# Performance work log

Hardware: AMD Instinct MI355X
Metric: run time of the kernel (lower is better)

Reference implementation:

```python
import jax, jax.numpy as jnp
import numpy as np

NUM_EXPERTS = 8
RANK = 16
TOP_K = 2
SCALING = 32.0 / RANK  # alpha / rank = 2.0
IN_F = 2048
OUT_F = 2048


def setup_inputs() -> dict:
    key = jax.random.key(0)
    k1, k2, k3, k4, k5 = jax.random.split(key, 5)
    B, T = 4, 2048
    x = jax.random.normal(k1, (B, T, IN_F), dtype=jnp.float32)
    # kaiming-uniform-ish scales
    bound_w = 1.0 / np.sqrt(IN_F)
    weight = jax.random.uniform(k2, (OUT_F, IN_F), jnp.float32, -bound_w, bound_w)
    lora_A = jax.random.uniform(k3, (NUM_EXPERTS, RANK, IN_F), jnp.float32, -bound_w, bound_w)
    # lora_B is zero-initialized in the module; use small random values so the
    # expert path is numerically non-trivial for kernel correctness testing.
    lora_B = 0.02 * jax.random.normal(k4, (NUM_EXPERTS, OUT_F, RANK), dtype=jnp.float32)
    router_w = jax.random.uniform(k5, (NUM_EXPERTS, IN_F), jnp.float32, -bound_w, bound_w)
    return {"x": x, "weight": weight, "lora_A": lora_A, "lora_B": lora_B, "router_w": router_w}


def reference(x, weight, lora_A, lora_B, router_w):
    B, T, D = x.shape
    N = B * T
    # base dense projection: [B,T,O]
    base = jnp.einsum('btd,od->bto', x, weight)
    # routing
    logits = jnp.einsum('btd,ed->bte', x, router_w)
    probs = jax.nn.softmax(logits, axis=-1)
    topk_vals, topk_idx = jax.lax.top_k(probs, TOP_K)          # [B,T,K]
    topk_vals = topk_vals / topk_vals.sum(axis=-1, keepdims=True)
    # dense per-token expert weights: zero for non-selected experts -> same math
    # as the per-k gather loop (top_k indices are distinct).
    w_dense = jnp.zeros((N, NUM_EXPERTS), dtype=x.dtype).at[
        jnp.arange(N)[:, None], topk_idx.reshape(N, TOP_K)
    ].set(topk_vals.reshape(N, TOP_K))                          # [N,E]
    x_flat = x.reshape(N, D)
    # low-rank expert path: Ax [N,E,r] is tiny (E*r=128), then weighted combine
    Ax = jnp.einsum('nd,erd->ner', x_flat, lora_A)
    expert_out = jnp.einsum('ner,ne,eor->no', Ax, w_dense, lora_B) * SCALING
    return base + expert_out.reshape(B, T, OUT_F)
```

## Files before the change

### kernel.cpp

```cpp
#include <hip/hip_runtime.h>
#include <hip/hip_bf16.h>
#include <stdint.h>

#define IN_F   2048
#define OUT_F  2048
#define NTOK   8192
#define KAUG   2176
#define RANKE  128
#define SCALING 2.0f
#define NT_MAIN 34

typedef float  f32x4 __attribute__((ext_vector_type(4)));
typedef __bf16 bf16x8 __attribute__((ext_vector_type(8)));

#define GLOAD(g, l) __builtin_amdgcn_global_load_lds(                                   \
    (const __attribute__((address_space(1))) unsigned int*)(g),                          \
    (__attribute__((address_space(3))) unsigned int*)(l), 16, 0, 0)
#define PIN()    asm volatile("" ::: "memory")
#define BAR()    __builtin_amdgcn_s_barrier()
#define WAITL()  asm volatile("s_waitcnt lgkmcnt(0)" ::: "memory")
#define WAITV0() asm volatile("s_waitcnt vmcnt(0)" ::: "memory")
#define WAITV5() asm volatile("s_waitcnt vmcnt(5)" ::: "memory")
#define WAITV8() asm volatile("s_waitcnt vmcnt(8)" ::: "memory")
#define SB0()    __builtin_amdgcn_sched_barrier(0)

__device__ __forceinline__ unsigned short f2b(float f) {
  union { float f; unsigned u; } v; v.f = f;
  return (unsigned short)((v.u + 0x7FFFu + ((v.u >> 16) & 1u)) >> 16);
}

__device__ __forceinline__ uint4 pack8(float4 a, float4 b) {
  uint4 p;
  p.x = f2b(a.x) | ((unsigned)f2b(a.y) << 16);
  p.y = f2b(a.z) | ((unsigned)f2b(a.w) << 16);
  p.z = f2b(b.x) | ((unsigned)f2b(b.y) << 16);
  p.w = f2b(b.z) | ((unsigned)f2b(b.w) << 16);
  return p;
}

__global__ __launch_bounds__(256)
void k_pre(const float* __restrict__ x, const float* __restrict__ rw,
           const float* __restrict__ wt, const float* __restrict__ lb,
           const float* __restrict__ la,
           unsigned short* __restrict__ Ap, float* __restrict__ wsc,
           unsigned short* __restrict__ Bp, unsigned short* __restrict__ Ac) {
  const int bid = blockIdx.x;
  const int t = threadIdx.x;

  if (bid >= 4096) {
    const int r0 = (bid - 4096) * 16;
    #pragma unroll
    for (int j = 0; j < 16; ++j) {
      int ch = j * 256 + t;
      int row = r0 + (ch >> 8), col8 = ch & 255;
      const float4* src = (const float4*)(la + (size_t)row * IN_F + col8 * 8);
      *(uint4*)(Ac + (size_t)row * IN_F + col8 * 8) = pack8(src[0], src[1]);
    }
    return;
  }
  if (bid >= 2048) {
    const int o = bid - 2048;
    const int c = t * 8;
    const float4* src = (const float4*)(wt + (size_t)o * IN_F + c);
    *(uint4*)(Bp + (size_t)o * KAUG + c) = pack8(src[0], src[1]);
    if (t < RANKE) {
      float v = lb[((size_t)(t >> 4) * OUT_F + o) * 16 + (t & 15)];
      Bp[(size_t)o * KAUG + IN_F + t] = f2b(v);
    }
    return;
  }

  const int w = t >> 6, l = t & 63;
  const int n0 = bid * 4;
  {
    const int n = n0 + w;
    const float4* src = (const float4*)(x + (size_t)n * IN_F);
    uint4* dst = (uint4*)(Ap + (size_t)n * KAUG);
    #pragma unroll
    for (int j = 0; j < 4; ++j) {
      int ch = j * 64 + l;
      dst[ch] = pack8(src[2 * ch], src[2 * ch + 1]);
    }
  }
  const int e = t & 7, p = t >> 3;
  float4 wreg[16];
  {
    const float4* wp = (const float4*)(rw + (size_t)e * IN_F + p * 64);
    #pragma unroll
    for (int j = 0; j < 16; ++j) wreg[j] = wp[j];
  }
  float s[4];
  #pragma unroll
  for (int ti = 0; ti < 4; ++ti) {
    const float4* xp = (const float4*)(x + (size_t)(n0 + ti) * IN_F + p * 64);
    float acc = 0.f;
    #pragma unroll
    for (int j = 0; j < 16; ++j) {
      float4 a = xp[j], b = wreg[j];
      acc += a.x * b.x + a.y * b.y + a.z * b.z + a.w * b.w;
    }
    s[ti] = acc;
  }
  #pragma unroll
  for (int ti = 0; ti < 4; ++ti) {
    s[ti] += __shfl_xor(s[ti], 8);
    s[ti] += __shfl_xor(s[ti], 16);
    s[ti] += __shfl_xor(s[ti], 32);
  }
  __shared__ float red[4][4][8];
  if (l < 8) {
    #pragma unroll
    for (int ti = 0; ti < 4; ++ti) red[ti][w][l] = s[ti];
  }
  __syncthreads();
  if (l < 8) {
    float tot = red[w][0][l] + red[w][1][l] + red[w][2][l] + red[w][3][l];
    float m = tot;
    m = fmaxf(m, __shfl_xor(m, 1));
    m = fmaxf(m, __shfl_xor(m, 2));
    m = fmaxf(m, __shfl_xor(m, 4));
    float ex = expf(tot - m);
    float dn = ex;
    dn += __shfl_xor(dn, 1);
    dn += __shfl_xor(dn, 2);
    dn += __shfl_xor(dn, 4);
    float prob = ex / dn;
    float v1 = prob; int i1 = l;
    #pragma unroll
    for (int msk = 1; msk <= 4; msk <<= 1) {
      float ov = __shfl_xor(v1, msk); int oi = __shfl_xor(i1, msk);
      if (ov > v1 || (ov == v1 && oi < i1)) { v1 = ov; i1 = oi; }
    }
    float v2 = (l == i1) ? -1.f : prob; int i2 = l;
    #pragma unroll
    for (int msk = 1; msk <= 4; msk <<= 1) {
      float ov = __shfl_xor(v2, msk); int oi = __shfl_xor(i2, msk);
      if (ov > v2 || (ov == v2 && oi < i2)) { v2 = ov; i2 = oi; }
    }
    float wsum = v1 + v2;
    float wv = (l == i1) ? (v1 / wsum) : ((l == i2) ? (v2 / wsum) : 0.f);
    wsc[(size_t)(n0 + w) * 8 + l] = wv * SCALING;
  }
}

__global__ __launch_bounds__(256)
void k_lora(const unsigned short* __restrict__ Ap, const unsigned short* __restrict__ Ac,
            const float* __restrict__ wsc, unsigned short* __restrict__ Vout) {
  __shared__ alignas(16) unsigned short LA[3 * 2048];
  __shared__ alignas(16) unsigned short LB[3 * 8192];
  const int t = threadIdx.x, bm = blockIdx.x;
  const int w = t >> 6, l = t & 63;
  const int lr = l & 15, lq = l >> 4, lx = l & 7;
  const unsigned short* Ablk = Ap + (size_t)bm * 32 * KAUG;
  const int rr = t >> 3, cs = t & 7;
  const int sc = cs ^ (rr & 7);

  f32x4 acc[2][2];
  #pragma unroll
  for (int i = 0; i < 2; ++i)
    #pragma unroll
    for (int j = 0; j < 2; ++j) acc[i][j] = f32x4{0.f, 0.f, 0.f, 0.f};

  auto stg = [&](int buf, int kt) {
    GLOAD(Ablk + (size_t)rr * KAUG + kt * 64 + sc * 8, LA + buf * 2048 + w * 512);
    #pragma unroll
    for (int r = 0; r < 4; ++r)
      GLOAD(Ac + (size_t)(r * 32 + rr) * IN_F + kt * 64 + sc * 8,
            LB + buf * 8192 + r * 2048 + w * 512);
  };

  const int as0 = (lq ^ lx) * 8, as1 = ((4 + lq) ^ lx) * 8;

  stg(0, 0); stg(1, 1);
  for (int kt = 0; kt < 32; ++kt) {
    if (kt == 31) { WAITV0(); } else { WAITV5(); }
    PIN(); BAR();
    if (kt + 2 < 32) stg((kt + 2) % 3, kt + 2);
    const int buf = kt % 3;
    bf16x8 aF[2][2], bF[2][2];
    #pragma unroll
    for (int mi = 0; mi < 2; ++mi) {
      aF[mi][0] = *(const bf16x8*)(LA + buf * 2048 + lr * 64 + mi * 1024 + as0);
      aF[mi][1] = *(const bf16x8*)(LA + buf * 2048 + lr * 64 + mi * 1024 + as1);
    }
    #pragma unroll
    for (int ni = 0; ni < 2; ++ni) {
      bF[ni][0] = *(const bf16x8*)(LB + buf * 8192 + w * 2048 + lr * 64 + ni * 1024 + as0);
      bF[ni][1] = *(const bf16x8*)(LB + buf * 8192 + w * 2048 + lr * 64 + ni * 1024 + as1);
    }
    #pragma unroll
    for (int mi = 0; mi < 2; ++mi)
      #pragma unroll
      for (int ni = 0; ni < 2; ++ni)
        #pragma unroll
        for (int ks = 0; ks < 2; ++ks)
          acc[mi][ni] = __builtin_amdgcn_mfma_f32_16x16x32_bf16(aF[mi][ks], bF[ni][ks], acc[mi][ni], 0, 0, 0);
  }

  #pragma unroll
  for (int mi = 0; mi < 2; ++mi)
    #pragma unroll
    for (int ni = 0; ni < 2; ++ni)
      #pragma unroll
      for (int j = 0; j < 4; ++j) {
        int row = bm * 32 + mi * 16 + lq * 4 + j;
        int col = w * 32 + ni * 16 + lr;
        float sg = wsc[row * 8 + (col >> 4)];
        Vout[(size_t)row * KAUG + col] = f2b(acc[mi][ni][j] * sg);
      }
}

__global__ __launch_bounds__(512, 2)
void k_main(const unsigned short* __restrict__ A, const unsigned short* __restrict__ B,
            float* __restrict__ out) {
  __shared__ alignas(16) unsigned short LDS[65536];

  const int tid = threadIdx.x;
  const int id = blockIdx.x;
  const int wg = (id & 7) * 32 + (id >> 3);
  const int bn = wg >> 5, bm = wg & 31;
  const int w = tid >> 6, l = tid & 63;
  const int wr = w >> 2, wc = w & 3;
  const int lr = l & 15, lq = l >> 4, lx = l & 7;

  const unsigned short* Ablk = A + (size_t)bm * 256 * KAUG;
  const unsigned short* Bblk = B + (size_t)bn * 256 * KAUG;

  const int rr = tid >> 3, cs = tid & 7;
  const int sc = cs ^ (rr & 7);
  const size_t gOfs = (size_t)rr * KAUG + sc * 8;
  unsigned short* const ldsW = LDS + w * 512;

  const int aoff = wr * 8192 + lr * 64;
  const int boff = (wc >> 1) * 8192 + (wc & 1) * 4096 + lr * 64;
  const int as0 = (lq ^ lx) * 8, as1 = ((4 + lq) ^ lx) * 8;

  f32x4 acc[8][4];
  #pragma unroll
  for (int i = 0; i < 8; ++i)
    #pragma unroll
    for (int j = 0; j < 4; ++j) acc[i][j] = f32x4{0.f, 0.f, 0.f, 0.f};
  bf16x8 aF[8][2], bF[4][2];

  auto stg = [&](int op, int buf, int h, int kt) {
    const unsigned short* g = (op ? Bblk : Ablk) + (size_t)(h * 128) * KAUG + (size_t)kt * 64 + gOfs;
    unsigned short* ld = ldsW + op * 32768 + buf * 16384 + h * 8192;
    GLOAD(g, ld);
    GLOAD(g + (size_t)64 * KAUG, ld + 4096);
  };

#define QUAD(mq, nq)                                                                     \
  do {                                                                                   \
    _Pragma("unroll") for (int mi_ = 0; mi_ < 4; ++mi_)                                  \
    _Pragma("unroll") for (int ni_ = 0; ni_ < 2; ++ni_)                                  \
    _Pragma("unroll") for (int ks_ = 0; ks_ < 2; ++ks_)                                  \
      acc[(mq)*4 + mi_][(nq)*2 + ni_] = __builtin_amdgcn_mfma_f32_16x16x32_bf16(         \
          aF[(mq)*4 + mi_][ks_], bF[(nq)*2 + ni_][ks_], acc[(mq)*4 + mi_][(nq)*2 + ni_], \
          0, 0, 0);                                                                      \
  } while (0)

  stg(0, 0, 0, 0); stg(0, 0, 1, 0); stg(1, 0, 0, 0); stg(1, 0, 1, 0);
  stg(0, 1, 0, 1); stg(0, 1, 1, 1); stg(1, 1, 0, 1); stg(1, 1, 1, 1);
  WAITV8(); PIN(); BAR();

  for (int t = 0; t < NT_MAIN; ++t) {
    const int buf = t & 1;
    #pragma unroll
    for (int mi = 0; mi < 4; ++mi) {
      aF[mi][0] = *(const bf16x8*)(LDS + buf * 16384 + aoff + mi * 1024 + as0);
      aF[mi][1] = *(const bf16x8*)(LDS + buf * 16384 + aoff + mi * 1024 + as1);
    }
    #pragma unroll
    for (int ni = 0; ni < 2; ++ni) {
      bF[ni][0] = *(const bf16x8*)(LDS + 32768 + buf * 16384 + boff + ni * 1024 + as0);
      bF[ni][1] = *(const bf16x8*)(LDS + 32768 + buf * 16384 + boff + ni * 1024 + as1);
    }
    PIN(); BAR(); WAITL(); SB0();
    __builtin_amdgcn_s_setprio(1); QUAD(0, 0); __builtin_amdgcn_s_setprio(0);
    PIN(); BAR();
    #pragma unroll
    for (int mi = 4; mi < 8; ++mi) {
      aF[mi][0] = *(const bf16x8*)(LDS + buf * 16384 + aoff + mi * 1024 + as0);
      aF[mi][1] = *(const bf16x8*)(LDS + buf * 16384 + aoff + mi * 1024 + as1);
    }
    #pragma unroll
    for (int ni = 2; ni < 4; ++ni) {
      bF[ni][0] = *(const bf16x8*)(LDS + 32768 + buf * 16384 + boff + ni * 1024 + as0);
      bF[ni][1] = *(const bf16x8*)(LDS + 32768 + buf * 16384 + boff + ni * 1024 + as1);
    }
    PIN(); BAR(); WAITL(); SB0();
    __builtin_amdgcn_s_setprio(1); QUAD(0, 1); __builtin_amdgcn_s_setprio(0);
    PIN(); BAR();
    if (t + 2 < NT_MAIN) { stg(0, buf, 0, t + 2); stg(1, buf, 0, t + 2); }
    PIN();
    __builtin_amdgcn_s_setprio(1); QUAD(1, 1); __builtin_amdgcn_s_setprio(0);
    PIN(); BAR();
    if (t + 2 < NT_MAIN) { stg(0, buf, 1, t + 2); stg(1, buf, 1, t + 2); }
    PIN();
    __builtin_amdgcn_s_setprio(1); QUAD(1, 0); __builtin_amdgcn_s_setprio(0);
    if (t + 2 < NT_MAIN) { WAITV8(); } else { WAITV0(); }
    PIN(); BAR();
  }
#undef QUAD

  #pragma unroll
  for (int mi = 0; mi < 8; ++mi)
    #pragma unroll
    for (int ni = 0; ni < 4; ++ni)
      #pragma unroll
      for (int j = 0; j < 4; ++j) {
        int row = bm * 256 + wr * 128 + mi * 16 + lq * 4 + j;
        int col = bn * 256 + wc * 64 + ni * 16 + lr;
        out[(size_t)row * OUT_F + col] = acc[mi][ni][j];
      }
}

extern "C" void kernel_launch(void* const* d_in, const int* in_sizes, int n_in,
                              void* d_out, int out_size, void* d_ws, size_t ws_size,
                              hipStream_t stream) {
  const float* x  = (const float*)d_in[0];
  const float* wt = (const float*)d_in[1];
  const float* la = (const float*)d_in[2];
  const float* lb = (const float*)d_in[3];
  const float* rw = (const float*)d_in[4];
  float* out = (float*)d_out;
  char* ws = (char*)d_ws;

  unsigned short* Ap  = (unsigned short*)ws;
  unsigned short* Bp  = (unsigned short*)(ws + 35651584);
  unsigned short* Ac  = (unsigned short*)(ws + 44564480);
  float*          wsc = (float*)(ws + 45088768);

  k_pre<<<4104, 256, 0, stream>>>(x, rw, wt, lb, la, Ap, wsc, Bp, Ac);
  k_lora<<<NTOK / 32, 256, 0, stream>>>(Ap, Ac, wsc, Ap + IN_F);
  k_main<<<256, 512, 0, stream>>>(Ap, Bp, out);
}
```

Measured before the change: 138.8 us.

## Switch main GEMM to K=32 tiles with four-stage LDS ring buffer

Restructures the main GEMM loop to use 32-wide K tiles instead of 64, with a 4-slot LDS ring buffer and prefetch depth of 3 instead of double-buffered 64-wide tiles. The LDS swizzle and global-to-LDS staging layout change to match the narrower tiles, and A/B loads are split across two phases per iteration. The aim is deeper latency hiding of global loads. In exchange the loop runs twice as many iterations, each with two barriers and fewer MFMAs per barrier, so synchronisation overhead grows.

Measured after the change: 142.9 us. +2.9%, slower.

```diff
diff --git a/kernel.cpp b/kernel.cpp
--- a/kernel.cpp
+++ b/kernel.cpp
@@ -8,7 +8,7 @@
 #define KAUG   2176
 #define RANKE  128
 #define SCALING 2.0f
-#define NT_MAIN 34
+#define NT32   68
 
 typedef float  f32x4 __attribute__((ext_vector_type(4)));
 typedef __bf16 bf16x8 __attribute__((ext_vector_type(8)));
@@ -20,6 +20,7 @@
 #define BAR()    __builtin_amdgcn_s_barrier()
 #define WAITL()  asm volatile("s_waitcnt lgkmcnt(0)" ::: "memory")
 #define WAITV0() asm volatile("s_waitcnt vmcnt(0)" ::: "memory")
+#define WAITV4() asm volatile("s_waitcnt vmcnt(4)" ::: "memory")
 #define WAITV5() asm volatile("s_waitcnt vmcnt(5)" ::: "memory")
 #define WAITV8() asm volatile("s_waitcnt vmcnt(8)" ::: "memory")
 #define SB0()    __builtin_amdgcn_sched_barrier(0)
@@ -221,88 +222,71 @@
   const int bn = wg >> 5, bm = wg & 31;
   const int w = tid >> 6, l = tid & 63;
   const int wr = w >> 2, wc = w & 3;
-  const int lr = l & 15, lq = l >> 4, lx = l & 7;
+  const int lr = l & 15;
 
   const unsigned short* Ablk = A + (size_t)bm * 256 * KAUG;
   const unsigned short* Bblk = B + (size_t)bn * 256 * KAUG;
 
-  const int rr = tid >> 3, cs = tid & 7;
-  const int sc = cs ^ (rr & 7);
-  const size_t gOfs = (size_t)rr * KAUG + sc * 8;
-  unsigned short* const ldsW = LDS + w * 512;
-
-  const int aoff = wr * 8192 + lr * 64;
-  const int boff = (wc >> 1) * 8192 + (wc & 1) * 4096 + lr * 64;
-  const int as0 = (lq ^ lx) * 8, as1 = ((4 + lq) ^ lx) * 8;
+  const int rr = tid >> 2, cs = tid & 3;
+  const size_t gOfs = (size_t)rr * KAUG + (size_t)((cs ^ ((rr >> 1) & 3)) * 8);
+
+  const int slotx = (l >> 4) ^ ((lr >> 1) & 3);
+  const int abase = (wr * 128 + lr) * 32 + slotx * 8;
+  const int bbase = 32768 + (wc * 64 + lr) * 32 + slotx * 8;
 
   f32x4 acc[8][4];
   #pragma unroll
   for (int i = 0; i < 8; ++i)
     #pragma unroll
     for (int j = 0; j < 4; ++j) acc[i][j] = f32x4{0.f, 0.f, 0.f, 0.f};
-  bf16x8 aF[8][2], bF[4][2];
-
-  auto stg = [&](int op, int buf, int h, int kt) {
-    const unsigned short* g = (op ? Bblk : Ablk) + (size_t)(h * 128) * KAUG + (size_t)kt * 64 + gOfs;
-    unsigned short* ld = ldsW + op * 32768 + buf * 16384 + h * 8192;
+  bf16x8 aF[8], bF[4];
+
+  auto stg = [&](int op, int bufm, int h, int kt) {
+    const unsigned short* g = (op ? Bblk : Ablk) + (size_t)(h * 128) * KAUG + (size_t)kt * 32 + gOfs;
+    unsigned short* ld = LDS + op * 32768 + bufm * 8192 + h * 4096 + w * 512;
     GLOAD(g, ld);
-    GLOAD(g + (size_t)64 * KAUG, ld + 4096);
   };
-
-#define QUAD(mq, nq)                                                                     \
-  do {                                                                                   \
-    _Pragma("unroll") for (int mi_ = 0; mi_ < 4; ++mi_)                                  \
-    _Pragma("unroll") for (int ni_ = 0; ni_ < 2; ++ni_)                                  \
-    _Pragma("unroll") for (int ks_ = 0; ks_ < 2; ++ks_)                                  \
-      acc[(mq)*4 + mi_][(nq)*2 + ni_] = __builtin_amdgcn_mfma_f32_16x16x32_bf16(         \
-          aF[(mq)*4 + mi_][ks_], bF[(nq)*2 + ni_][ks_], acc[(mq)*4 + mi_][(nq)*2 + ni_], \
-          0, 0, 0);                                                                      \
-  } while (0)
 
   stg(0, 0, 0, 0); stg(0, 0, 1, 0); stg(1, 0, 0, 0); stg(1, 0, 1, 0);
   stg(0, 1, 0, 1); stg(0, 1, 1, 1); stg(1, 1, 0, 1); stg(1, 1, 1, 1);
+  stg(0, 2, 0, 2); stg(0, 2, 1, 2); stg(1, 2, 0, 2); stg(1, 2, 1, 2);
   WAITV8(); PIN(); BAR();
 
-  for (int t = 0; t < NT_MAIN; ++t) {
-    const int buf = t & 1;
-    #pragma unroll
-    for (int mi = 0; mi < 4; ++mi) {
-      aF[mi][0] = *(const bf16x8*)(LDS + buf * 16384 + aoff + mi * 1024 + as0);
-      aF[mi][1] = *(const bf16x8*)(LDS + buf * 16384 + aoff + mi * 1024 + as1);
-    }
-    #pragma unroll
-    for (int ni = 0; ni < 2; ++ni) {
-      bF[ni][0] = *(const bf16x8*)(LDS + 32768 + buf * 16384 + boff + ni * 1024 + as0);
-      bF[ni][1] = *(const bf16x8*)(LDS + 32768 + buf * 16384 + boff + ni * 1024 + as1);
-    }
+  for (int t = 0; t < NT32; ++t) {
+    const int buf = t & 3, sb = (t + 3) & 3;
+    const int ab = buf * 8192 + abase, bb = buf * 8192 + bbase;
+    #pragma unroll
+    for (int mi = 0; mi < 4; ++mi) aF[mi] = *(const bf16x8*)(LDS + ab + mi * 512);
+    #pragma unroll
+    for (int ni = 0; ni < 4; ++ni) bF[ni] = *(const bf16x8*)(LDS + bb + ni * 512);
+    if (t + 3 < NT32) { stg(0, sb, 0, t + 3); stg(0, sb, 1, t + 3); }
     PIN(); BAR(); WAITL(); SB0();
-    __builtin_amdgcn_s_setprio(1); QUAD(0, 0); __builtin_amdgcn_s_setprio(0);
+    __builtin_amdgcn_s_setprio(1);
+    #pragma unroll
+    for (int mi = 0; mi < 4; ++mi)
+      #pragma unroll
+      for (int ni = 0; ni < 4; ++ni)
+        acc[mi][ni] = __builtin_amdgcn_mfma_f32_16x16x32_bf16(aF[mi], bF[ni], acc[mi][ni], 0, 0, 0);
+    __builtin_amdgcn_s_setprio(0);
     PIN(); BAR();
     #pragma unroll
-    for (int mi = 4; mi < 8; ++mi) {
-      aF[mi][0] = *(const bf16x8*)(LDS + buf * 16384 + aoff + mi * 1024 + as0);
-      aF[mi][1] = *(const bf16x8*)(LDS + buf * 16384 + aoff + mi * 1024 + as1);
-    }
-    #pragma unroll
-    for (int ni = 2; ni < 4; ++ni) {
-      bF[ni][0] = *(const bf16x8*)(LDS + 32768 + buf * 16384 + boff + ni * 1024 + as0);
-      bF[ni][1] = *(const bf16x8*)(LDS + 32768 + buf * 16384 + boff + ni * 1024 + as1);
-    }
+    for (int mi = 4; mi < 8; ++mi) aF[mi] = *(const bf16x8*)(LDS + ab + mi * 512);
+    if (t + 3 < NT32) { stg(1, sb, 0, t + 3); stg(1, sb, 1, t + 3); }
     PIN(); BAR(); WAITL(); SB0();
-    __builtin_amdgcn_s_setprio(1); QUAD(0, 1); __builtin_amdgcn_s_setprio(0);
+    __builtin_amdgcn_s_setprio(1);
+    #pragma unroll
+    for (int mi = 4; mi < 8; ++mi)
+      #pragma unroll
+      for (int ni = 0; ni < 4; ++ni)
+        acc[mi][ni] = __builtin_amdgcn_mfma_f32_16x16x32_bf16(aF[mi], bF[ni], acc[mi][ni], 0, 0, 0);
+    __builtin_amdgcn_s_setprio(0);
+    if (t + 3 < NT32) { WAITV8(); }
+    else if (t + 2 < NT32) { WAITV4(); }
+    else if (t + 1 < NT32) { WAITV0(); }
     PIN(); BAR();
-    if (t + 2 < NT_MAIN) { stg(0, buf, 0, t + 2); stg(1, buf, 0, t + 2); }
-    PIN();
-    __builtin_amdgcn_s_setprio(1); QUAD(1, 1); __builtin_amdgcn_s_setprio(0);
-    PIN(); BAR();
-    if (t + 2 < NT_MAIN) { stg(0, buf, 1, t + 2); stg(1, buf, 1, t + 2); }
-    PIN();
-    __builtin_amdgcn_s_setprio(1); QUAD(1, 0); __builtin_amdgcn_s_setprio(0);
-    if (t + 2 < NT_MAIN) { WAITV8(); } else { WAITV0(); }
-    PIN(); BAR();
-  }
-#undef QUAD
-
+  }
+
+  const int lq = l >> 4;
   #pragma unroll
   for (int mi = 0; mi < 8; ++mi)
     #pragma unroll
```

## Restructure GEMM pipeline with staggered A/B prefetch and reduced fragment registers

Applied to the files above, without the earlier changes.

The main bf16 GEMM loop is unrolled by two k-tiles and reschedules the global-to-LDS loads. A halves for the next tile are issued early within the current tile, and B halves two tiles ahead. A fragments are reloaded per M-quad so only four A fragments are live, which cuts register pressure. The pre-kernel also folds the x-to-bf16 conversion into the router dot-product loop so x is read once instead of twice. The tighter buffer reuse depends on the barrier and waitcnt ordering being correct, so a misplaced wait could race on LDS.

Result: slower. 195.4 us (+40.7%).

```diff
diff --git a/kernel.cpp b/kernel.cpp
--- a/kernel.cpp
+++ b/kernel.cpp
@@ -8,7 +8,8 @@
 #define KAUG   2176
 #define RANKE  128
 #define SCALING 2.0f
-#define NT_MAIN 34
+#define NT64   34
+#define NITER  17
 
 typedef float  f32x4 __attribute__((ext_vector_type(4)));
 typedef __bf16 bf16x8 __attribute__((ext_vector_type(8)));
@@ -19,9 +20,10 @@
 #define PIN()    asm volatile("" ::: "memory")
 #define BAR()    __builtin_amdgcn_s_barrier()
 #define WAITL()  asm volatile("s_waitcnt lgkmcnt(0)" ::: "memory")
+#define WAITL8() asm volatile("s_waitcnt lgkmcnt(8)" ::: "memory")
 #define WAITV0() asm volatile("s_waitcnt vmcnt(0)" ::: "memory")
+#define WAITV4() asm volatile("s_waitcnt vmcnt(4)" ::: "memory")
 #define WAITV5() asm volatile("s_waitcnt vmcnt(5)" ::: "memory")
-#define WAITV8() asm volatile("s_waitcnt vmcnt(8)" ::: "memory")
 #define SB0()    __builtin_amdgcn_sched_barrier(0)
 
 __device__ __forceinline__ unsigned short f2b(float f) {
@@ -72,16 +74,6 @@
 
   const int w = t >> 6, l = t & 63;
   const int n0 = bid * 4;
-  {
-    const int n = n0 + w;
-    const float4* src = (const float4*)(x + (size_t)n * IN_F);
-    uint4* dst = (uint4*)(Ap + (size_t)n * KAUG);
-    #pragma unroll
-    for (int j = 0; j < 4; ++j) {
-      int ch = j * 64 + l;
-      dst[ch] = pack8(src[2 * ch], src[2 * ch + 1]);
-    }
-  }
   const int e = t & 7, p = t >> 3;
   float4 wreg[16];
   {
@@ -93,11 +85,15 @@
   #pragma unroll
   for (int ti = 0; ti < 4; ++ti) {
     const float4* xp = (const float4*)(x + (size_t)(n0 + ti) * IN_F + p * 64);
+    uint4* dst = (uint4*)(Ap + (size_t)(n0 + ti) * KAUG + p * 64);
     float acc = 0.f;
+    float4 prev;
     #pragma unroll
     for (int j = 0; j < 16; ++j) {
       float4 a = xp[j], b = wreg[j];
       acc += a.x * b.x + a.y * b.y + a.z * b.z + a.w * b.w;
+      if (j & 1) { if (e == ti) dst[j >> 1] = pack8(prev, a); }
+      else prev = a;
     }
     s[ti] = acc;
   }
@@ -226,79 +222,124 @@
   const unsigned short* Ablk = A + (size_t)bm * 256 * KAUG;
   const unsigned short* Bblk = B + (size_t)bn * 256 * KAUG;
 
-  const int rr = tid >> 3, cs = tid & 7;
-  const int sc = cs ^ (rr & 7);
-  const size_t gOfs = (size_t)rr * KAUG + sc * 8;
+  const size_t gofs0 = (size_t)(tid >> 3) * KAUG + (size_t)(((tid & 7) ^ ((tid >> 3) & 7)) * 8);
+  const size_t gofs1 = (size_t)((tid + 512) >> 3) * KAUG +
+                       (size_t)((((tid + 512) & 7) ^ (((tid + 512) >> 3) & 7)) * 8);
   unsigned short* const ldsW = LDS + w * 512;
 
-  const int aoff = wr * 8192 + lr * 64;
-  const int boff = (wc >> 1) * 8192 + (wc & 1) * 4096 + lr * 64;
-  const int as0 = (lq ^ lx) * 8, as1 = ((4 + lq) ^ lx) * 8;
+  const int arow = wr * 128 + lr, brow = wc * 64 + lr;
+  const int sl0 = (lq ^ lx) * 8, sl1 = ((4 + lq) ^ lx) * 8;
 
   f32x4 acc[8][4];
   #pragma unroll
   for (int i = 0; i < 8; ++i)
     #pragma unroll
     for (int j = 0; j < 4; ++j) acc[i][j] = f32x4{0.f, 0.f, 0.f, 0.f};
-  bf16x8 aF[8][2], bF[4][2];
-
-  auto stg = [&](int op, int buf, int h, int kt) {
-    const unsigned short* g = (op ? Bblk : Ablk) + (size_t)(h * 128) * KAUG + (size_t)kt * 64 + gOfs;
-    unsigned short* ld = ldsW + op * 32768 + buf * 16384 + h * 8192;
-    GLOAD(g, ld);
-    GLOAD(g + (size_t)64 * KAUG, ld + 4096);
+  bf16x8 aF[4][2], bF[4][2];
+
+  auto stage = [&](int isB, int half, int kt) {
+    if (kt >= NT64) return;
+    const unsigned short* g = (isB ? Bblk : Ablk) + (size_t)(half * 128) * KAUG + (size_t)kt * 64;
+    unsigned short* ld = ldsW + isB * 32768 + (kt & 1) * 16384 + half * 8192;
+    GLOAD(g + gofs0, ld);
+    GLOAD(g + gofs1, ld + 4096);
   };
 
-#define QUAD(mq, nq)                                                                     \
+#define QUAD(MQ, NQ)                                                                     \
   do {                                                                                   \
     _Pragma("unroll") for (int mi_ = 0; mi_ < 4; ++mi_)                                  \
     _Pragma("unroll") for (int ni_ = 0; ni_ < 2; ++ni_)                                  \
     _Pragma("unroll") for (int ks_ = 0; ks_ < 2; ++ks_)                                  \
-      acc[(mq)*4 + mi_][(nq)*2 + ni_] = __builtin_amdgcn_mfma_f32_16x16x32_bf16(         \
-          aF[(mq)*4 + mi_][ks_], bF[(nq)*2 + ni_][ks_], acc[(mq)*4 + mi_][(nq)*2 + ni_], \
+      acc[(MQ)*4 + mi_][(NQ)*2 + ni_] = __builtin_amdgcn_mfma_f32_16x16x32_bf16(         \
+          aF[mi_][ks_], bF[(NQ)*2 + ni_][ks_], acc[(MQ)*4 + mi_][(NQ)*2 + ni_],          \
           0, 0, 0);                                                                      \
   } while (0)
 
-  stg(0, 0, 0, 0); stg(0, 0, 1, 0); stg(1, 0, 0, 0); stg(1, 0, 1, 0);
-  stg(0, 1, 0, 1); stg(0, 1, 1, 1); stg(1, 1, 0, 1); stg(1, 1, 1, 1);
-  WAITV8(); PIN(); BAR();
-
-  for (int t = 0; t < NT_MAIN; ++t) {
-    const int buf = t & 1;
+  stage(1, 0, 0); stage(1, 1, 0); stage(0, 0, 0); stage(0, 1, 0);
+  stage(1, 0, 1); stage(1, 1, 1);
+  WAITV4(); PIN(); BAR();
+
+  for (int i = 0; i < NITER; ++i) {
+    const int k1 = 2 * i + 1;
+    const int a0 = arow * 64,   b0 = 32768 + brow * 64;
+    const int a1 = a0 + 16384,  b1 = b0 + 16384;
+
     #pragma unroll
     for (int mi = 0; mi < 4; ++mi) {
-      aF[mi][0] = *(const bf16x8*)(LDS + buf * 16384 + aoff + mi * 1024 + as0);
-      aF[mi][1] = *(const bf16x8*)(LDS + buf * 16384 + aoff + mi * 1024 + as1);
+      aF[mi][0] = *(const bf16x8*)(LDS + a0 + mi * 1024 + sl0);
+      aF[mi][1] = *(const bf16x8*)(LDS + a0 + mi * 1024 + sl1);
     }
     #pragma unroll
     for (int ni = 0; ni < 2; ++ni) {
-      bF[ni][0] = *(const bf16x8*)(LDS + 32768 + buf * 16384 + boff + ni * 1024 + as0);
-      bF[ni][1] = *(const bf16x8*)(LDS + 32768 + buf * 16384 + boff + ni * 1024 + as1);
-    }
-    PIN(); BAR(); WAITL(); SB0();
+      bF[ni][0] = *(const bf16x8*)(LDS + b0 + ni * 1024 + sl0);
+      bF[ni][1] = *(const bf16x8*)(LDS + b0 + ni * 1024 + sl1);
+    }
+    stage(0, 0, k1);
+    PIN(); WAITL8(); PIN(); BAR(); WAITL(); SB0();
     __builtin_amdgcn_s_setprio(1); QUAD(0, 0); __builtin_amdgcn_s_setprio(0);
     PIN(); BAR();
     #pragma unroll
-    for (int mi = 4; mi < 8; ++mi) {
-      aF[mi][0] = *(const bf16x8*)(LDS + buf * 16384 + aoff + mi * 1024 + as0);
-      aF[mi][1] = *(const bf16x8*)(LDS + buf * 16384 + aoff + mi * 1024 + as1);
-    }
-    #pragma unroll
     for (int ni = 2; ni < 4; ++ni) {
-      bF[ni][0] = *(const bf16x8*)(LDS + 32768 + buf * 16384 + boff + ni * 1024 + as0);
-      bF[ni][1] = *(const bf16x8*)(LDS + 32768 + buf * 16384 + boff + ni * 1024 + as1);
-    }
+      bF[ni][0] = *(const bf16x8*)(LDS + b0 + ni * 1024 + sl0);
+      bF[ni][1] = *(const bf16x8*)(LDS + b0 + ni * 1024 + sl1);
+    }
+    stage(0, 1, k1);
     PIN(); BAR(); WAITL(); SB0();
     __builtin_amdgcn_s_setprio(1); QUAD(0, 1); __builtin_amdgcn_s_setprio(0);
     PIN(); BAR();
-    if (t + 2 < NT_MAIN) { stg(0, buf, 0, t + 2); stg(1, buf, 0, t + 2); }
+    #pragma unroll
+    for (int mi = 0; mi < 4; ++mi) {
+      aF[mi][0] = *(const bf16x8*)(LDS + a0 + (mi + 4) * 1024 + sl0);
+      aF[mi][1] = *(const bf16x8*)(LDS + a0 + (mi + 4) * 1024 + sl1);
+    }
+    stage(1, 0, k1 + 1);
+    PIN(); BAR(); WAITL(); SB0();
+    __builtin_amdgcn_s_setprio(1); QUAD(1, 1); __builtin_amdgcn_s_setprio(0);
+    PIN(); BAR();
+    stage(1, 1, k1 + 1);
+    PIN(); BAR();
+    __builtin_amdgcn_s_setprio(1); QUAD(1, 0); __builtin_amdgcn_s_setprio(0);
     PIN();
+    if (i == NITER - 1) { WAITV0(); } else { WAITV4(); }
+    PIN(); BAR();
+
+    #pragma unroll
+    for (int mi = 0; mi < 4; ++mi) {
+      aF[mi][0] = *(const bf16x8*)(LDS + a1 + mi * 1024 + sl0);
+      aF[mi][1] = *(const bf16x8*)(LDS + a1 + mi * 1024 + sl1);
+    }
+    #pragma unroll
+    for (int ni = 0; ni < 2; ++ni) {
+      bF[ni][0] = *(const bf16x8*)(LDS + b1 + ni * 1024 + sl0);
+      bF[ni][1] = *(const bf16x8*)(LDS + b1 + ni * 1024 + sl1);
+    }
+    stage(0, 0, k1 + 1);
+    PIN(); WAITL8(); PIN(); BAR(); WAITL(); SB0();
+    __builtin_amdgcn_s_setprio(1); QUAD(0, 0); __builtin_amdgcn_s_setprio(0);
+    PIN(); BAR();
+    #pragma unroll
+    for (int ni = 2; ni < 4; ++ni) {
+      bF[ni][0] = *(const bf16x8*)(LDS + b1 + ni * 1024 + sl0);
+      bF[ni][1] = *(const bf16x8*)(LDS + b1 + ni * 1024 + sl1);
+    }
+    stage(0, 1, k1 + 1);
+    PIN(); BAR(); WAITL(); SB0();
+    __builtin_amdgcn_s_setprio(1); QUAD(0, 1); __builtin_amdgcn_s_setprio(0);
+    PIN(); BAR();
+    #pragma unroll
+    for (int mi = 0; mi < 4; ++mi) {
+      aF[mi][0] = *(const bf16x8*)(LDS + a1 + (mi + 4) * 1024 + sl0);
+      aF[mi][1] = *(const bf16x8*)(LDS + a1 + (mi + 4) * 1024 + sl1);
+    }
+    stage(1, 0, k1 + 2);
+    PIN(); BAR(); WAITL(); SB0();
     __builtin_amdgcn_s_setprio(1); QUAD(1, 1); __builtin_amdgcn_s_setprio(0);
     PIN(); BAR();
-    if (t + 2 < NT_MAIN) { stg(0, buf, 1, t + 2); stg(1, buf, 1, t + 2); }
+    stage(1, 1, k1 + 2);
+    PIN(); BAR();
+    __builtin_amdgcn_s_setprio(1); QUAD(1, 0); __builtin_amdgcn_s_setprio(0);
     PIN();
-    __builtin_amdgcn_s_setprio(1); QUAD(1, 0); __builtin_amdgcn_s_setprio(0);
-    if (t + 2 < NT_MAIN) { WAITV8(); } else { WAITV0(); }
+    if (i == NITER - 1) { WAITV0(); } else { WAITV4(); }
     PIN(); BAR();
   }
 #undef QUAD
```
